# Kernel optimization log

Measured on AMD Instinct MI355X. Metric: run time of the kernel, lower is better.

Reference implementation:

```python
import jax, jax.numpy as jnp
import numpy as np

RADIUS = 0.45


def _square_distance(src, dst):
    # [B,N,C] x [B,M,C] -> [B,N,M] squared Euclidean distances
    d = -2.0 * jnp.einsum('bnc,bmc->bnm', src, dst)
    d = d + jnp.sum(src * src, -1)[:, :, None]
    d = d + jnp.sum(dst * dst, -1)[:, None, :]
    return d


def _query_ball(radius, nsample, xyz):
    # faithful to torch query_ball_point: mark out-of-radius as N, sort, take nsample, fill with first
    B, N, _ = xyz.shape
    sqr = _square_distance(xyz, xyz)  # [B,N,N]
    idx = jnp.where(sqr > radius * radius, N,
                    jnp.arange(N, dtype=jnp.int32)[None, None, :])
    idx = jnp.sort(idx, axis=-1)[:, :, :nsample]  # [B,N,nsample]
    first = idx[:, :, :1]
    return jnp.where(idx == N, first, idx)


def _gather(points, idx):
    # points [B,N,C], idx [B,S,K] -> [B,S,K,C]
    B = points.shape[0]
    return points[jnp.arange(B)[:, None, None], idx]


def _mlp2(g, W1, b1, W2, b2):
    # g: [B,S,K,Cin]; 1x1 conv2d == per-point matmul; relu each layer
    h = jax.nn.relu(jnp.einsum('bskc,oc->bsko', g, W1) + b1)
    h = jax.nn.relu(jnp.einsum('bski,oi->bsko', h, W2) + b2)
    return jnp.max(h, axis=2)  # max over neighbors K -> [B,S,Cout]


def setup_inputs() -> dict:
    key = jax.random.key(0)
    ks = jax.random.split(key, 13)
    B, N = 8, 2048
    s = 0.1
    return {
        'x': jax.random.uniform(ks[0], (B, N, 3), dtype=jnp.float32),
        'W1a': jax.random.normal(ks[1], (32, 3), dtype=jnp.float32) * s,
        'b1a': jnp.zeros((32,), jnp.float32),
        'W2a': jax.random.normal(ks[2], (64, 32), dtype=jnp.float32) * s,
        'b2a': jnp.zeros((64,), jnp.float32),
        'W1b': jax.random.normal(ks[3], (64, 3), dtype=jnp.float32) * s,
        'b1b': jnp.zeros((64,), jnp.float32),
        'W2b': jax.random.normal(ks[4], (128, 64), dtype=jnp.float32) * s,
        'b2b': jnp.zeros((128,), jnp.float32),
        'Wc1': jax.random.normal(ks[5], (64, 3), dtype=jnp.float32) * s,
        'bc1': jnp.zeros((64,), jnp.float32),
        'Wc2': jax.random.normal(ks[6], (256, 128), dtype=jnp.float32) * s,
        'bc2': jnp.zeros((256,), jnp.float32),
    }


def reference(x, W1a, b1a, W2a, b2a, W1b, b1b, W2b, b2b, Wc1, bc1, Wc2, bc2):
    # branch 1: ball query (nsample=64) -> gather -> 1x1 MLP (3->32->64) -> max-pool
    idx1 = _query_ball(RADIUS, 64, x)
    g1 = _mlp2(_gather(x, idx1), W1a, b1a, W2a, b2a)  # [B,N,64]
    g1 = jnp.transpose(g1, (0, 2, 1))                 # [B,64,N]

    # point-wise conv1d 3->64 on raw coords
    xf = jax.nn.relu(jnp.einsum('bnc,oc->bon', x, Wc1) + bc1[None, :, None])
    xf = jnp.concatenate([xf, g1], axis=1)            # [B,128,N]
    xf = jax.nn.relu(jnp.einsum('bcn,oc->bon', xf, Wc2) + bc2[None, :, None])  # [B,256,N]

    # branch 2: ball query (nsample=128) -> gather -> 1x1 MLP (3->64->128) -> max-pool
    idx2 = _query_ball(RADIUS, 128, x)
    g2 = _mlp2(_gather(x, idx2), W1b, b1b, W2b, b2b)  # [B,N,128]
    g2 = jnp.transpose(g2, (0, 2, 1))                 # [B,128,N]

    return jnp.concatenate([xf, g2], axis=1)          # [B,384,N]
```

## Files before the change

### kernel.cpp

```cpp
#include <hip/hip_runtime.h>
#include <hip/hip_fp16.h>
#include <cstdint>

#define NPTS 2048
#define NB 8
#define R2C 0.2025f

__device__ __forceinline__ float fmul(float a, float b) { return __fmul_rn(a, b); }
__device__ __forceinline__ float fadd(float a, float b) { return __fadd_rn(a, b); }

__device__ __forceinline__ uint hmax2u(uint a, uint b) {
    uint r;
    asm volatile("v_pk_max_f16 %0, %1, %2" : "=v"(r) : "v"(a), "v"(b));
    return r;
}
__device__ __forceinline__ float lo_f(uint u) {
    __half h = __ushort_as_half((unsigned short)(u & 0xffff));
    return __half2float(h);
}
__device__ __forceinline__ float hi_f(uint u) {
    __half h = __ushort_as_half((unsigned short)(u >> 16));
    return __half2float(h);
}

__global__ __launch_bounds__(512, 4) void k_features(
    const float* __restrict__ X,
    const float* __restrict__ W1a, const float* __restrict__ b1a,
    const float* __restrict__ W2a, const float* __restrict__ b2a,
    const float* __restrict__ W1b, const float* __restrict__ b1b,
    const float* __restrict__ W2b, const float* __restrict__ b2b,
    const float* __restrict__ Wc1, const float* __restrict__ bc1,
    __half* __restrict__ fa, __half* __restrict__ fb, float* __restrict__ v)
{
    __shared__ float fat[64 * 33];
    __shared__ float fbt[64 * 67];
    int tid = threadIdx.x;
    int q = __builtin_amdgcn_readfirstlane(tid >> 6);
    int lane = tid & 63;
    int pbase = blockIdx.x * 64;
    int p = pbase + lane;
    int b = p >> 11, i = p & 2047;

    float x0 = X[p * 3 + 0], x1 = X[p * 3 + 1], x2 = X[p * 3 + 2];

    float h[64];
#pragma unroll
    for (int o = 0; o < 32; ++o)
        h[o] = fmaxf(0.f, x0 * W1a[o * 3] + x1 * W1a[o * 3 + 1] + x2 * W1a[o * 3 + 2] + b1a[o]);
#pragma unroll
    for (int oo = 0; oo < 8; oo += 2) {
        int o = q * 8 + oo;
        float a0 = b2a[o], a1 = b2a[o + 1];
#pragma unroll
        for (int k = 0; k < 32; ++k) {
            a0 = fmaf(h[k], W2a[o * 32 + k], a0);
            a1 = fmaf(h[k], W2a[(o + 1) * 32 + k], a1);
        }
        __half2 hh = __floats2half2_rn(fmaxf(0.f, a0), fmaxf(0.f, a1));
        fat[lane * 33 + q * 4 + (oo >> 1)] = *(float*)&hh;
    }
#pragma unroll
    for (int o = 0; o < 64; ++o)
        h[o] = fmaxf(0.f, x0 * W1b[o * 3] + x1 * W1b[o * 3 + 1] + x2 * W1b[o * 3 + 2] + b1b[o]);
#pragma unroll
    for (int oo = 0; oo < 16; oo += 2) {
        int o = q * 16 + oo;
        float a0 = b2b[o], a1 = b2b[o + 1];
#pragma unroll
        for (int k = 0; k < 64; ++k) {
            a0 = fmaf(h[k], W2b[o * 64 + k], a0);
            a1 = fmaf(h[k], W2b[(o + 1) * 64 + k], a1);
        }
        __half2 hh = __floats2half2_rn(fmaxf(0.f, a0), fmaxf(0.f, a1));
        fbt[lane * 67 + q * 8 + (oo >> 1)] = *(float*)&hh;
    }
    float* vb = v + (size_t)b * 128 * NPTS + i;
#pragma unroll
    for (int oo = 0; oo < 8; ++oo) {
        int o = q * 8 + oo;
        vb[(size_t)o * NPTS] =
            fmaxf(0.f, x0 * Wc1[o * 3] + x1 * Wc1[o * 3 + 1] + x2 * Wc1[o * 3 + 2] + bc1[o]);
    }
    __syncthreads();

    uint* fau = (uint*)fa;
#pragma unroll
    for (int r = 0; r < 4; ++r) {
        int idx = r * 512 + tid;
        int pt = idx >> 5, j = idx & 31;
        fau[((size_t)(pbase + pt)) * 32 + j] = *(uint*)&fat[pt * 33 + j];
    }
    uint* fbu = (uint*)fb;
#pragma unroll
    for (int r = 0; r < 8; ++r) {
        int idx = r * 512 + tid;
        int pt = idx >> 6, j = idx & 63;
        fbu[((size_t)(pbase + pt)) * 64 + j] = *(uint*)&fbt[pt * 67 + j];
    }
}

__global__ __launch_bounds__(1024) void k_neighbors(
    const float* __restrict__ X, const __half* __restrict__ fa,
    const __half* __restrict__ fb, float* __restrict__ v, float* __restrict__ out)
{
    __shared__ float4 xs4[NPTS];
    __shared__ unsigned short nbr[16][128];
    __shared__ float g1t[64][17];
    __shared__ float g2t[128][17];
    int tid = threadIdx.x;
    int wid = tid >> 6, lane = tid & 63;
    int b = blockIdx.x & 7;
    int i0 = (blockIdx.x >> 3) * 16;
    int i = i0 + wid;

    const float* Xb = X + (size_t)b * NPTS * 3;
    for (int t = tid; t < NPTS; t += 1024) {
        float y0 = Xb[3 * t], y1 = Xb[3 * t + 1], y2 = Xb[3 * t + 2];
        float mm = fadd(fadd(fmul(y0, y0), fmul(y1, y1)), fmul(y2, y2));
        xs4[t] = make_float4(y0, y1, y2, mm);
    }
    __syncthreads();

    float4 cc = xs4[i];
    float n0 = cc.x, n1 = cc.y, n2 = cc.z, nn = cc.w;

    unsigned long long myword = 0;
    for (int w = 0; w < 32; ++w) {
        float4 y = xs4[(w << 6) | lane];
        float dot = fadd(fadd(fmul(n0, y.x), fmul(n1, y.y)), fmul(n2, y.z));
        float d   = fadd(fadd(fmul(-2.0f, dot), nn), y.w);
        unsigned long long bm = __ballot(!(d > R2C));
        if (lane == w) myword = bm;
    }

    int cnt = (lane < 32) ? __popcll(myword) : 0;
    int incl = cnt;
#pragma unroll
    for (int d = 1; d < 32; d <<= 1) {
        int t = __shfl_up(incl, d, 64);
        if (lane >= d) incl += t;
    }
    int pre = incl - cnt;
    if (lane < 32 && cnt && pre < 128) {
        unsigned long long word = myword;
        int r = pre;
        while (word && r < 128) {
            int pb = __builtin_ctzll(word);
            word &= word - 1;
            nbr[wid][r++] = (unsigned short)((lane << 6) | pb);
        }
    }
    int total = __shfl(incl, 31, 64);
    int c1 = min(total, 64);
    int c2 = min(total, 128);
    __syncthreads();

    {
        const uint4* fab = (const uint4*)(fa + (size_t)b * NPTS * 64);
        int g = lane >> 3, c8 = lane & 7;
        int cl = c1 - 1;
        uint4 r[8];
#pragma unroll
        for (int j = 0; j < 8; ++j) {
            int idx = j * 8 + g; idx = idx > cl ? cl : idx;
            int row = nbr[wid][idx];
            r[j] = fab[row * 8 + c8];
        }
        uint acc0 = 0, acc1 = 0, acc2 = 0, acc3 = 0;
#pragma unroll
        for (int j = 0; j < 8; ++j) {
            acc0 = hmax2u(acc0, r[j].x);
            acc1 = hmax2u(acc1, r[j].y);
            acc2 = hmax2u(acc2, r[j].z);
            acc3 = hmax2u(acc3, r[j].w);
        }
#pragma unroll
        for (int s = 8; s < 64; s <<= 1) {
            acc0 = hmax2u(acc0, (uint)__shfl_xor((int)acc0, s, 64));
            acc1 = hmax2u(acc1, (uint)__shfl_xor((int)acc1, s, 64));
            acc2 = hmax2u(acc2, (uint)__shfl_xor((int)acc2, s, 64));
            acc3 = hmax2u(acc3, (uint)__shfl_xor((int)acc3, s, 64));
        }
        if (g == 0) {
            uint a[4] = {acc0, acc1, acc2, acc3};
#pragma unroll
            for (int k = 0; k < 4; ++k) {
                g1t[8 * c8 + 2 * k][wid]     = lo_f(a[k]);
                g1t[8 * c8 + 2 * k + 1][wid] = hi_f(a[k]);
            }
        }
    }
    {
        const uint4* fbb = (const uint4*)(fb + (size_t)b * NPTS * 128);
        int g = lane >> 4, c8 = lane & 15;
        int cl = c2 - 1;
        uint acc0 = 0, acc1 = 0, acc2 = 0, acc3 = 0;
#pragma unroll
        for (int jo = 0; jo < 32; jo += 8) {
            uint4 r[8];
#pragma unroll
            for (int jj = 0; jj < 8; ++jj) {
                int idx = (jo + jj) * 4 + g; idx = idx > cl ? cl : idx;
                int row = nbr[wid][idx];
                r[jj] = fbb[row * 16 + c8];
            }
#pragma unroll
            for (int jj = 0; jj < 8; ++jj) {
                acc0 = hmax2u(acc0, r[jj].x);
                acc1 = hmax2u(acc1, r[jj].y);
                acc2 = hmax2u(acc2, r[jj].z);
                acc3 = hmax2u(acc3, r[jj].w);
            }
        }
#pragma unroll
        for (int s = 16; s < 64; s <<= 1) {
            acc0 = hmax2u(acc0, (uint)__shfl_xor((int)acc0, s, 64));
            acc1 = hmax2u(acc1, (uint)__shfl_xor((int)acc1, s, 64));
            acc2 = hmax2u(acc2, (uint)__shfl_xor((int)acc2, s, 64));
            acc3 = hmax2u(acc3, (uint)__shfl_xor((int)acc3, s, 64));
        }
        if (g == 0) {
            uint a[4] = {acc0, acc1, acc2, acc3};
#pragma unroll
            for (int k = 0; k < 4; ++k) {
                g2t[8 * c8 + 2 * k][wid]     = lo_f(a[k]);
                g2t[8 * c8 + 2 * k + 1][wid] = hi_f(a[k]);
            }
        }
    }
    __syncthreads();

    {
        int ch = tid >> 4, pt = tid & 15;
        v[((size_t)b * 128 + 64 + ch) * NPTS + i0 + pt] = g1t[ch][pt];
    }
#pragma unroll
    for (int r = 0; r < 2; ++r) {
        int idx = r * 1024 + tid;
        int ch = idx >> 4, pt = idx & 15;
        out[((size_t)b * 384 + 256 + ch) * NPTS + i0 + pt] = g2t[ch][pt];
    }
}

__global__ __launch_bounds__(256) void k_conv2(
    const float* __restrict__ v, const float* __restrict__ Wc2,
    const float* __restrict__ bc2, float* __restrict__ out)
{
    __shared__ float vs[128 * 32];
    __shared__ float ws[256 * 33];
    int b = blockIdx.x & 7;
    int nt = (blockIdx.x >> 3) << 5;
    int t = threadIdx.x;
    int n_t = t & 3, o_t = t >> 2;

    const float* vb = v + (size_t)b * 128 * NPTS + nt;
#pragma unroll
    for (int r = 0; r < 4; ++r) {
        int j = r * 256 + t; int k = j >> 3, n4 = j & 7;
        *(float4*)&vs[k * 32 + n4 * 4] = *(const float4*)(vb + (size_t)k * NPTS + n4 * 4);
    }

    float acc[4][8];
#pragma unroll
    for (int r = 0; r < 4; ++r) {
        float bb = bc2[o_t * 4 + r];
#pragma unroll
        for (int n = 0; n < 8; ++n) acc[r][n] = bb;
    }

    for (int kc = 0; kc < 128; kc += 32) {
        __syncthreads();
#pragma unroll
        for (int r = 0; r < 8; ++r) {
            int j = r * 256 + t; int o = j >> 3, c = j & 7;
            float4 wv = *(const float4*)(Wc2 + (size_t)o * 128 + kc + c * 4);
            ws[o * 33 + c * 4 + 0] = wv.x;
            ws[o * 33 + c * 4 + 1] = wv.y;
            ws[o * 33 + c * 4 + 2] = wv.z;
            ws[o * 33 + c * 4 + 3] = wv.w;
        }
        __syncthreads();
#pragma unroll 4
        for (int kk = 0; kk < 32; ++kk) {
            float4 va = *(float4*)&vs[(kc + kk) * 32 + n_t * 8];
            float4 vb4 = *(float4*)&vs[(kc + kk) * 32 + n_t * 8 + 4];
            float vv[8] = {va.x, va.y, va.z, va.w, vb4.x, vb4.y, vb4.z, vb4.w};
            float ww[4];
#pragma unroll
            for (int r = 0; r < 4; ++r) ww[r] = ws[(o_t * 4 + r) * 33 + kk];
#pragma unroll
            for (int r = 0; r < 4; ++r)
#pragma unroll
                for (int n = 0; n < 8; ++n)
                    acc[r][n] = fmaf(ww[r], vv[n], acc[r][n]);
        }
    }

    float* ob = out + ((size_t)b * 384 + o_t * 4) * NPTS + nt + n_t * 8;
#pragma unroll
    for (int r = 0; r < 4; ++r) {
        float4 s0, s1;
        s0.x = fmaxf(0.f, acc[r][0]); s0.y = fmaxf(0.f, acc[r][1]);
        s0.z = fmaxf(0.f, acc[r][2]); s0.w = fmaxf(0.f, acc[r][3]);
        s1.x = fmaxf(0.f, acc[r][4]); s1.y = fmaxf(0.f, acc[r][5]);
        s1.z = fmaxf(0.f, acc[r][6]); s1.w = fmaxf(0.f, acc[r][7]);
        *(float4*)(ob + (size_t)r * NPTS) = s0;
        *(float4*)(ob + (size_t)r * NPTS + 4) = s1;
    }
}

extern "C" void kernel_launch(void* const* d_in, const int* in_sizes, int n_in,
                              void* d_out, int out_size, void* d_ws, size_t ws_size,
                              hipStream_t stream) {
    const float* X   = (const float*)d_in[0];
    const float* W1a = (const float*)d_in[1];
    const float* b1a = (const float*)d_in[2];
    const float* W2a = (const float*)d_in[3];
    const float* b2a = (const float*)d_in[4];
    const float* W1b = (const float*)d_in[5];
    const float* b1b = (const float*)d_in[6];
    const float* W2b = (const float*)d_in[7];
    const float* b2b = (const float*)d_in[8];
    const float* Wc1 = (const float*)d_in[9];
    const float* bc1 = (const float*)d_in[10];
    const float* Wc2 = (const float*)d_in[11];
    const float* bc2 = (const float*)d_in[12];
    float* out = (float*)d_out;

    __half* fa = (__half*)d_ws;
    __half* fb = fa + (size_t)NB * NPTS * 64;
    float*  v  = (float*)(fb + (size_t)NB * NPTS * 128);

    k_features<<<NB * NPTS / 64, 512, 0, stream>>>(X, W1a, b1a, W2a, b2a,
                                                   W1b, b1b, W2b, b2b, Wc1, bc1,
                                                   fa, fb, v);
    k_neighbors<<<NB * NPTS / 16, 1024, 0, stream>>>(X, fa, fb, v, out);
    k_conv2<<<NB * (NPTS / 32), 256, 0, stream>>>(v, Wc2, bc2, out);
}
```

Baseline: 176.6 us.

## Split neighbor search and feature pooling into separate kernels

Splits the fused neighbor kernel into a ballot kernel that writes neighbor lists and counts to global memory, and a pooling kernel with smaller 512-thread blocks and launch bounds that allow higher occupancy for the gather-max phase. The pooling kernel also issues 16 outstanding gathers per batch instead of 8 for more memory-level parallelism. In exchange it adds an extra kernel launch and a global round trip for neighbor indices, and raises register pressure from the larger load batch.

```diff
diff --git a/kernel.cpp b/kernel.cpp
--- a/kernel.cpp
+++ b/kernel.cpp
@@ -99,14 +99,13 @@
     }
 }
 
-__global__ __launch_bounds__(1024) void k_neighbors(
-    const float* __restrict__ X, const __half* __restrict__ fa,
-    const __half* __restrict__ fb, float* __restrict__ v, float* __restrict__ out)
+__global__ __launch_bounds__(1024) void k_ballot(
+    const float* __restrict__ X, unsigned short* __restrict__ nbrg,
+    int* __restrict__ cnt)
 {
     __shared__ float4 xs4[NPTS];
     __shared__ unsigned short nbr[16][128];
-    __shared__ float g1t[64][17];
-    __shared__ float g2t[128][17];
+    __shared__ int cts[16];
     int tid = threadIdx.x;
     int wid = tid >> 6, lane = tid & 63;
     int b = blockIdx.x & 7;
@@ -133,15 +132,15 @@
         if (lane == w) myword = bm;
     }
 
-    int cnt = (lane < 32) ? __popcll(myword) : 0;
-    int incl = cnt;
+    int c = (lane < 32) ? __popcll(myword) : 0;
+    int incl = c;
 #pragma unroll
     for (int d = 1; d < 32; d <<= 1) {
         int t = __shfl_up(incl, d, 64);
         if (lane >= d) incl += t;
     }
-    int pre = incl - cnt;
-    if (lane < 32 && cnt && pre < 128) {
+    int pre = incl - c;
+    if (lane < 32 && c && pre < 128) {
         unsigned long long word = myword;
         int r = pre;
         while (word && r < 128) {
@@ -151,9 +150,35 @@
         }
     }
     int total = __shfl(incl, 31, 64);
-    int c1 = min(total, 64);
-    int c2 = min(total, 128);
-    __syncthreads();
+    if (lane == 0) cts[wid] = total;
+    __syncthreads();
+
+    uint* ng = (uint*)(nbrg + ((size_t)b * NPTS + i0) * 128);
+    ng[tid] = *(uint*)&nbr[tid >> 6][(tid & 63) * 2];
+    if (tid < 16) cnt[(size_t)b * NPTS + i0 + tid] = cts[tid];
+}
+
+__global__ __launch_bounds__(512, 4) void k_pool(
+    const __half* __restrict__ fa, const __half* __restrict__ fb,
+    const unsigned short* __restrict__ nbrg, const int* __restrict__ cnt,
+    float* __restrict__ v, float* __restrict__ out)
+{
+    __shared__ uint nbrl[8][64];
+    __shared__ float g1t[64][9];
+    __shared__ float g2t[128][9];
+    int tid = threadIdx.x;
+    int wid = __builtin_amdgcn_readfirstlane(tid >> 6);
+    int lane = tid & 63;
+    int b = blockIdx.x & 7;
+    int i0 = (blockIdx.x >> 3) * 8;
+    int i = i0 + wid;
+
+    nbrl[tid >> 6][tid & 63] = ((const uint*)(nbrg + ((size_t)b * NPTS + i0) * 128))[tid];
+    int total = max(cnt[(size_t)b * NPTS + i], 1);
+    int c1 = min(total, 64), c2 = min(total, 128);
+    __syncthreads();
+
+    const unsigned short* list = (const unsigned short*)nbrl[wid];
 
     {
         const uint4* fab = (const uint4*)(fa + (size_t)b * NPTS * 64);
@@ -163,8 +188,7 @@
 #pragma unroll
         for (int j = 0; j < 8; ++j) {
             int idx = j * 8 + g; idx = idx > cl ? cl : idx;
-            int row = nbr[wid][idx];
-            r[j] = fab[row * 8 + c8];
+            r[j] = fab[(int)list[idx] * 8 + c8];
         }
         uint acc0 = 0, acc1 = 0, acc2 = 0, acc3 = 0;
 #pragma unroll
@@ -196,16 +220,15 @@
         int cl = c2 - 1;
         uint acc0 = 0, acc1 = 0, acc2 = 0, acc3 = 0;
 #pragma unroll
-        for (int jo = 0; jo < 32; jo += 8) {
-            uint4 r[8];
-#pragma unroll
-            for (int jj = 0; jj < 8; ++jj) {
+        for (int jo = 0; jo < 32; jo += 16) {
+            uint4 r[16];
+#pragma unroll
+            for (int jj = 0; jj < 16; ++jj) {
                 int idx = (jo + jj) * 4 + g; idx = idx > cl ? cl : idx;
-                int row = nbr[wid][idx];
-                r[jj] = fbb[row * 16 + c8];
+                r[jj] = fbb[(int)list[idx] * 16 + c8];
             }
 #pragma unroll
-            for (int jj = 0; jj < 8; ++jj) {
+            for (int jj = 0; jj < 16; ++jj) {
                 acc0 = hmax2u(acc0, r[jj].x);
                 acc1 = hmax2u(acc1, r[jj].y);
                 acc2 = hmax2u(acc2, r[jj].z);
@@ -231,13 +254,13 @@
     __syncthreads();
 
     {
-        int ch = tid >> 4, pt = tid & 15;
+        int ch = tid >> 3, pt = tid & 7;
         v[((size_t)b * 128 + 64 + ch) * NPTS + i0 + pt] = g1t[ch][pt];
     }
 #pragma unroll
     for (int r = 0; r < 2; ++r) {
-        int idx = r * 1024 + tid;
-        int ch = idx >> 4, pt = idx & 15;
+        int idx = r * 512 + tid;
+        int ch = idx >> 3, pt = idx & 7;
         out[((size_t)b * 384 + 256 + ch) * NPTS + i0 + pt] = g2t[ch][pt];
     }
 }
@@ -330,10 +353,13 @@
     __half* fa = (__half*)d_ws;
     __half* fb = fa + (size_t)NB * NPTS * 64;
     float*  v  = (float*)(fb + (size_t)NB * NPTS * 128);
+    unsigned short* nbrg = (unsigned short*)(v + (size_t)NB * 128 * NPTS);
+    int* cnt = (int*)(nbrg + (size_t)NB * NPTS * 128);
 
     k_features<<<NB * NPTS / 64, 512, 0, stream>>>(X, W1a, b1a, W2a, b2a,
                                                    W1b, b1b, W2b, b2b, Wc1, bc1,
                                                    fa, fb, v);
-    k_neighbors<<<NB * NPTS / 16, 1024, 0, stream>>>(X, fa, fb, v, out);
+    k_ballot<<<NB * NPTS / 16, 1024, 0, stream>>>(X, nbrg, cnt);
+    k_pool<<<NB * NPTS / 8, 512, 0, stream>>>(fa, fb, nbrg, cnt, v, out);
     k_conv2<<<NB * (NPTS / 32), 256, 0, stream>>>(v, Wc2, bc2, out);
 }
```

After: 178.7 us. No clear change (+1.1%).
